# Performance work log

Hardware: AMD Instinct MI355X
Metric: run time of the kernel (lower is better)

The kernel has to match this reference:

```python
import jax, jax.numpy as jnp
import numpy as np

B, C, N, K = 8, 128, 16384, 8


def setup_inputs() -> dict:
    key = jax.random.key(0)
    ks = jax.random.split(key, 20)
    s = 1.0 / np.sqrt(C)
    def mat(k_, shape, scale):
        return jax.random.normal(k_, shape, jnp.float32) * scale
    return {
        "x": jax.random.normal(ks[0], (B, C, N, 1), jnp.float32),
        "logits": jax.random.normal(ks[1], (B, N), jnp.float32),
        "Wq1": mat(ks[2], (C, C), s), "Wk1": mat(ks[3], (C, C), s), "Wv1": mat(ks[4], (C, C), s),
        "Wq2": mat(ks[5], (C, C), s), "Wk2": mat(ks[6], (C, C), s), "Wv2": mat(ks[7], (C, C), s),
        "Wq3": mat(ks[8], (C, C), s), "Wk3": mat(ks[9], (C, C), s), "Wv3": mat(ks[10], (C, C), s),
        "ln_w": jnp.ones((C,), jnp.float32), "ln_b": jnp.zeros((C,), jnp.float32),
        "conv0_w": mat(ks[11], (C, C), s), "conv0_b": jnp.zeros((C,), jnp.float32),
        "bn_w": jnp.ones((C,), jnp.float32), "bn_b": jnp.zeros((C,), jnp.float32),
        "fc1_w": mat(ks[12], (C // 2, C), s), "fc1_b": jnp.zeros((C // 2,), jnp.float32),
        "fc2_w": mat(ks[13], (C, C // 2), 1.0 / np.sqrt(C // 2)), "fc2_b": jnp.zeros((C,), jnp.float32),
        "k": K,
    }


def _transformer(f, Wq, Wk, Wv):
    # f: [B, C, n] ; 1x1 convs over channel dim
    q = jnp.einsum('oc,bcn->bon', Wq, f)
    kk = jnp.einsum('oc,bcn->bon', Wk, f)
    v = jnp.einsum('oc,bcn->bon', Wv, f)
    temp = jnp.sqrt(jnp.asarray(f.shape[1], f.dtype))
    attn = jax.nn.softmax(jnp.einsum('bcn,bdn->bcd', q / temp, kk), axis=-1)  # [B,C,C]
    return jnp.einsum('bcd,bdn->bcn', attn, v)


def _layernorm_over_c(f, w, b):
    # f: [B, C, n]; original transposes to [B, n, C], LayerNorm(C, eps=1e-6), back
    ft = jnp.swapaxes(f, 1, 2)
    mu = ft.mean(-1, keepdims=True)
    var = ft.var(-1, keepdims=True)
    ft = (ft - mu) * jax.lax.rsqrt(var + 1e-6) * w + b
    return jnp.swapaxes(ft, 1, 2)


def reference(x, logits, Wq1, Wk1, Wv1, Wq2, Wk2, Wv2, Wq3, Wk3, Wv3,
              ln_w, ln_b, conv0_w, conv0_b, bn_w, bn_b, fc1_w, fc1_b, fc2_w, fc2_b, k):
    # --- tanh-threshold binning into k buckets ---
    w = jnp.tanh(logits)                       # [B, N]
    flag = 2.0 / k
    lows = -1.0 + flag * jnp.arange(k, dtype=x.dtype)   # [k]
    highs = lows + flag
    wb = w[None, :, :]                         # [1, B, N]
    # transforto0_1: in (l, r], and original zeros stay zero
    masks = ((wb > lows[:, None, None]) & (wb <= highs[:, None, None]) & (wb != 0)).astype(x.dtype)  # [k,B,N]
    nums = masks.sum(-1)                       # [k, B]
    nums = jnp.where(nums == 0, 1.0, nums)

    x2 = x[..., 0]                             # [B, C, N]
    # masked segment pooling (mean per bin), no channel-broadcast repeat
    pooled = jnp.einsum('bcn,kbn->bck', x2, masks)        # [B, C, k]
    feature = pooled / nums.T[:, None, :]                 # [B, C, k]

    # --- three tiny attention blocks with residual + LN ---
    for Wq, Wk, Wv in ((Wq1, Wk1, Wv1), (Wq2, Wk2, Wv2), (Wq3, Wk3, Wv3)):
        out = _transformer(feature, Wq, Wk, Wv) + feature
        feature = _layernorm_over_c(out, ln_w, ln_b)

    # --- scatter-add reconstruction: sum_i mask_i*x + mask_i*level_i ---
    total = masks.sum(0)                                  # [B, N]
    recon = x2 * total[:, None, :] + jnp.einsum('bck,kbn->bcn', feature, masks)
    result = recon[..., None]                             # [B, C, N, 1]

    # --- SE block ---
    mu_i = result.mean(axis=(2, 3), keepdims=True)
    var_i = result.var(axis=(2, 3), keepdims=True)
    h = (result - mu_i) * jax.lax.rsqrt(var_i + 1e-5)     # InstanceNorm2d
    mu_b = h.mean(axis=(0, 2, 3), keepdims=True)
    var_b = h.var(axis=(0, 2, 3), keepdims=True)
    h = (h - mu_b) * jax.lax.rsqrt(var_b + 1e-5)          # BatchNorm2d (batch stats)
    h = h * bn_w[None, :, None, None] + bn_b[None, :, None, None]
    h = jax.nn.gelu(h, approximate=False)
    conv = jnp.einsum('oc,bcnp->bonp', conv0_w, h) + conv0_b[None, :, None, None]
    sq = conv.reshape(conv.shape[0], conv.shape[1], -1).mean(-1)   # [B, C]
    f1 = jax.nn.gelu(sq @ fc1_w.T + fc1_b, approximate=False)
    f2 = jax.nn.sigmoid(f1 @ fc2_w.T + fc2_b)
    return conv * f2[:, :, None, None]
```

## Files before the change

kernel.cpp:

```cpp
#include <hip/hip_runtime.h>
#include <math.h>

#define Bdim 8
#define Cdim 128
#define Ndim 16384
#define Kdim 8

typedef __attribute__((ext_vector_type(8))) short short8;
typedef __attribute__((ext_vector_type(4))) float f32x4;

__device__ __forceinline__ unsigned rne16(float x) {
  unsigned u = __float_as_uint(x);
  return (u + 0x7FFFu + ((u >> 16) & 1u)) >> 16;
}

__global__ void __launch_bounds__(256) k_prep(
    const float* __restrict__ W, unsigned short* __restrict__ Wh,
    unsigned short* __restrict__ Wl, unsigned short* __restrict__ Whs,
    unsigned short* __restrict__ Wls,
    const float* __restrict__ p0, const float* __restrict__ p1, const float* __restrict__ p2,
    const float* __restrict__ p3, const float* __restrict__ p4, const float* __restrict__ p5,
    const float* __restrict__ p6, const float* __restrict__ p7, const float* __restrict__ p8,
    unsigned short* __restrict__ Wbf, int* __restrict__ cnt, float* __restrict__ gmean) {
  int blk = blockIdx.x, t = threadIdx.x;
  if (blk < 64) {
    int idx = blk * 256 + t;
    int o = idx >> 7, c = idx & 127;
    float v = W[idx];
    unsigned u = __float_as_uint(v);
    unsigned rh = (u + 0x7FFFu + ((u >> 16) & 1u)) & 0xFFFF0000u;
    float vh = __uint_as_float(rh);
    float r = v - vh;
    unsigned u2 = __float_as_uint(r);
    unsigned rl = (u2 + 0x7FFFu + ((u2 >> 16) & 1u)) >> 16;
    unsigned short hs = (unsigned short)(rh >> 16);
    unsigned short ls = (unsigned short)rl;
    Wh[idx] = hs;
    Wl[idx] = ls;
    int pos = o * 128 + (((c >> 3) ^ (o & 7)) << 3) + (c & 7);
    Whs[pos] = hs;
    Wls[pos] = ls;
    if (blk == 0 && t < Bdim * Kdim) cnt[t] = 0;
    if (blk < 4) gmean[blk * 256 + t] = 0.f;
  } else {
    int m = (blk - 64) >> 6;
    int i = ((blk - 64) & 63) * 256 + t;
    const float* mp = m == 0 ? p0 : m == 1 ? p1 : m == 2 ? p2 : m == 3 ? p3 : m == 4 ? p4
                    : m == 5 ? p5 : m == 6 ? p6 : m == 7 ? p7 : p8;
    Wbf[m * 16384 + i] = (unsigned short)rne16(mp[i]);
  }
}

__global__ void __launch_bounds__(256) k_bin(const float* __restrict__ logits,
                                             signed char* __restrict__ kbin,
                                             int* __restrict__ cnt) {
  __shared__ int h[Kdim];
  int tid = threadIdx.x;
  if (tid < Kdim) h[tid] = 0;
  __syncthreads();
  int idx = blockIdx.x * 256 + tid;
  int b = idx >> 14;
  float w = tanhf(logits[idx]);
  int kb = -1;
#pragma unroll
  for (int j = 0; j < Kdim; ++j) {
    float lo = -1.0f + 0.25f * (float)j;
    float hi = lo + 0.25f;
    if (w > lo && w <= hi && w != 0.0f) kb = j;
  }
  kbin[idx] = (signed char)kb;
  if (kb >= 0) atomicAdd(&h[kb], 1);
  __syncthreads();
  if (tid < Kdim) atomicAdd(&cnt[b * Kdim + tid], h[tid]);
}

__global__ void __launch_bounds__(256) k_pool(const float* __restrict__ x,
                                              const signed char* __restrict__ kbin,
                                              float* __restrict__ pooled,
                                              float* __restrict__ sxx) {
  int bc = blockIdx.x;
  int b = bc >> 7;
  const float4* xr = (const float4*)(x + (size_t)bc * Ndim);
  const char4* kr = (const char4*)(kbin + b * Ndim);
  float acc[Kdim];
#pragma unroll
  for (int j = 0; j < Kdim; ++j) acc[j] = 0.f;
  float s2 = 0.f;
  int tid = threadIdx.x;
  for (int n4 = tid; n4 < Ndim / 4; n4 += 256) {
    float4 v = xr[n4];
    char4 kb = kr[n4];
    float ve[4] = {v.x, v.y, v.z, v.w};
    signed char ke[4] = {kb.x, kb.y, kb.z, kb.w};
#pragma unroll
    for (int e = 0; e < 4; ++e) {
      float xv = ve[e];
      int kv = ke[e];
      if (kv >= 0) s2 += xv * xv;
#pragma unroll
      for (int j = 0; j < Kdim; ++j) acc[j] += (kv == j) ? xv : 0.f;
    }
  }
#pragma unroll
  for (int off = 32; off > 0; off >>= 1) {
#pragma unroll
    for (int j = 0; j < Kdim; ++j) acc[j] += __shfl_down(acc[j], off);
    s2 += __shfl_down(s2, off);
  }
  __shared__ float red[4][Kdim + 1];
  int wv = tid >> 6, ln = tid & 63;
  if (ln == 0) {
#pragma unroll
    for (int j = 0; j < Kdim; ++j) red[wv][j] = acc[j];
    red[wv][Kdim] = s2;
  }
  __syncthreads();
  if (tid < Kdim) pooled[bc * Kdim + tid] = red[0][tid] + red[1][tid] + red[2][tid] + red[3][tid];
  if (tid == Kdim) sxx[bc] = red[0][Kdim] + red[1][Kdim] + red[2][Kdim] + red[3][Kdim];
}

__global__ void __launch_bounds__(256) k_warm(const unsigned short* __restrict__ Wbf,
                                              float* __restrict__ dummy) {
  int g = blockIdx.x >> 3;
  int t = threadIdx.x;
  int idx = g * 256 + t;
  uint4 v = ((const uint4*)Wbf)[idx];
  float s = (float)(v.x ^ v.y ^ v.z ^ v.w);
#pragma unroll
  for (int off = 32; off > 0; off >>= 1) s += __shfl_down(s, off);
  if ((t & 63) == 0) dummy[blockIdx.x * 4 + (t >> 6)] = s;
}

__global__ void __launch_bounds__(1024) k_xform(
    const float* __restrict__ pooled, const int* __restrict__ cnt,
    const float* __restrict__ sxx, const unsigned short* __restrict__ Wbf,
    const float* __restrict__ ln_w, const float* __restrict__ ln_b,
    float* __restrict__ feat, float* __restrict__ mu_i, float* __restrict__ rs_i,
    float* __restrict__ ratio) {
  __shared__ float f_l[Kdim][132], q_l[Kdim][132], kk_l[Kdim][132], v_l[Kdim][132];
  __shared__ unsigned short fTh[16][132], fTl[16][132];
  __shared__ float part[Kdim][Kdim][Cdim];
  __shared__ float pm[Kdim][Cdim], ps[Kdim][Cdim];
  __shared__ float lnw_l[Cdim], lnb_l[Cdim];
  __shared__ float cnt_raw[Kdim], cnt_div[Kdim];
  __shared__ float redA[Kdim][2], redB[Kdim][2];
  int b = blockIdx.x, tid = threadIdx.x;
  int c_ = tid & 127, h_ = tid >> 7;
  int o8 = tid >> 3, j8 = tid & 7;
  int wid = tid >> 6, lane = tid & 63;
  int l15 = lane & 15, lg = lane >> 4;
  const float inv_temp = 0.08838834764831845f;

  if (tid < Kdim) {
    int cc = cnt[b * Kdim + tid];
    cnt_raw[tid] = (float)cc;
    cnt_div[tid] = (float)(cc == 0 ? 1 : cc);
  }
  if (tid >= 128 && tid < 256) lnw_l[tid - 128] = ln_w[tid - 128];
  if (tid >= 256 && tid < 384) lnb_l[tid - 256] = ln_b[tid - 256];
  __syncthreads();
  {
    float fv = pooled[(b * Cdim + o8) * Kdim + j8] / cnt_div[j8];
    f_l[j8][o8] = fv;
    unsigned hi = rne16(fv);
    fTh[j8][o8] = (unsigned short)hi;
    fTl[j8][o8] = (unsigned short)rne16(fv - __uint_as_float(hi << 16));
  }
  float t_carry = 0.f;
  float sv[16];
  float mloc = 0.f;
  for (int layer = 0; layer < 3; ++layer) {
    if (layer > 0) {
      float S1 = redA[h_][0] + redA[h_][1];
      float S2 = redB[h_][0] + redB[h_][1];
      float mu = S1 * (1.f / Cdim);
      float var = S2 * (1.f / Cdim) - mu * mu;
      float rs = rsqrtf(var + 1e-6f);
      float fv = (t_carry - mu) * rs * lnw_l[c_] + lnb_l[c_];
      f_l[h_][c_] = fv;
      unsigned hi = rne16(fv);
      fTh[h_][c_] = (unsigned short)hi;
      fTl[h_][c_] = (unsigned short)rne16(fv - __uint_as_float(hi << 16));
    }
    __syncthreads();
    for (int job = wid; job < 24; job += 16) {
      int m = job >> 3, ot = job & 7;
      const unsigned short* A = Wbf + (size_t)(layer * 3 + m) * 16384 + (ot * 16 + l15) * 128;
      f32x4 acc = (f32x4){0.f, 0.f, 0.f, 0.f};
#pragma unroll
      for (int ks = 0; ks < 4; ++ks) {
        int kbase = ks * 32 + lg * 8;
        short8 a = *(const short8*)(A + kbase);
        short8 bh = *(const short8*)&fTh[l15][kbase];
        short8 bl = *(const short8*)&fTl[l15][kbase];
        acc = __builtin_amdgcn_mfma_f32_16x16x32_bf16(a, bh, acc, 0, 0, 0);
        acc = __builtin_amdgcn_mfma_f32_16x16x32_bf16(a, bl, acc, 0, 0, 0);
      }
      if (l15 < 8) {
#pragma unroll
        for (int r = 0; r < 4; ++r) {
          int o = ot * 16 + lg * 4 + r;
          float v = acc[r];
          if (m == 0) q_l[l15][o] = v * inv_temp;
          else if (m == 1) kk_l[l15][o] = v;
          else v_l[l15][o] = v;
        }
      }
    }
    __syncthreads();
    {
      int d0 = h_ * 16;
      float qv[8];
#pragma unroll
      for (int j = 0; j < 8; ++j) qv[j] = q_l[j][c_];
#pragma unroll
      for (int dd = 0; dd < 16; ++dd) sv[dd] = 0.f;
#pragma unroll
      for (int j = 0; j < 8; ++j) {
#pragma unroll
        for (int d4 = 0; d4 < 4; ++d4) {
          float4 k4 = *(const float4*)&kk_l[j][d0 + d4 * 4];
          sv[d4 * 4 + 0] = fmaf(qv[j], k4.x, sv[d4 * 4 + 0]);
          sv[d4 * 4 + 1] = fmaf(qv[j], k4.y, sv[d4 * 4 + 1]);
          sv[d4 * 4 + 2] = fmaf(qv[j], k4.z, sv[d4 * 4 + 2]);
          sv[d4 * 4 + 3] = fmaf(qv[j], k4.w, sv[d4 * 4 + 3]);
        }
      }
      mloc = sv[0];
#pragma unroll
      for (int dd = 1; dd < 16; ++dd) mloc = fmaxf(mloc, sv[dd]);
      float sl = 0.f;
#pragma unroll
      for (int dd = 0; dd < 16; ++dd) {
        sv[dd] = expf(sv[dd] - mloc);
        sl += sv[dd];
      }
      pm[h_][c_] = mloc;
      ps[h_][c_] = sl;
    }
    __syncthreads();
    {
      float M = pm[0][c_];
#pragma unroll
      for (int hh = 1; hh < 8; ++hh) M = fmaxf(M, pm[hh][c_]);
      float S = 0.f;
#pragma unroll
      for (int hh = 0; hh < 8; ++hh) S += ps[hh][c_] * expf(pm[hh][c_] - M);
      float fac = expf(mloc - M) / S;
#pragma unroll
      for (int dd = 0; dd < 16; ++dd) sv[dd] *= fac;
      int d0 = h_ * 16;
#pragma unroll
      for (int j = 0; j < 8; ++j) {
        float po = 0.f;
#pragma unroll
        for (int d4 = 0; d4 < 4; ++d4) {
          float4 v4 = *(const float4*)&v_l[j][d0 + d4 * 4];
          po = fmaf(sv[d4 * 4 + 0], v4.x, po);
          po = fmaf(sv[d4 * 4 + 1], v4.y, po);
          po = fmaf(sv[d4 * 4 + 2], v4.z, po);
          po = fmaf(sv[d4 * 4 + 3], v4.w, po);
        }
        part[h_][j][c_] = po;
      }
    }
    __syncthreads();
    {
      float t = f_l[h_][c_];
#pragma unroll
      for (int hh = 0; hh < 8; ++hh) t += part[hh][h_][c_];
      t_carry = t;
      float s1 = t, s2 = t * t;
#pragma unroll
      for (int off = 32; off > 0; off >>= 1) {
        s1 += __shfl_xor(s1, off);
        s2 += __shfl_xor(s2, off);
      }
      int wv = (tid >> 6) & 1;
      if ((tid & 63) == 0) { redA[h_][wv] = s1; redB[h_][wv] = s2; }
    }
    __syncthreads();
  }
  {
    float S1 = redA[h_][0] + redA[h_][1];
    float S2 = redB[h_][0] + redB[h_][1];
    float mu = S1 * (1.f / Cdim);
    float var = S2 * (1.f / Cdim) - mu * mu;
    float rs = rsqrtf(var + 1e-6f);
    f_l[h_][c_] = (t_carry - mu) * rs * lnw_l[c_] + lnb_l[c_];
  }
  __syncthreads();
  if (tid < Cdim) {
    int c = tid;
    float S1 = 0.f, S2c = 0.f;
#pragma unroll
    for (int j = 0; j < Kdim; ++j) {
      float pl = pooled[(b * Cdim + c) * Kdim + j];
      float fe = f_l[j][c];
      feat[(b * Cdim + c) * Kdim + j] = fe;
      S1 += pl + cnt_raw[j] * fe;
      S2c += 2.f * pl * fe + cnt_raw[j] * fe * fe;
    }
    float S2 = sxx[b * Cdim + c] + S2c;
    float mu = S1 * (1.f / Ndim);
    float var = S2 * (1.f / Ndim) - mu * mu;
    float rs = rsqrtf(var + 1e-5f);
    mu_i[b * Cdim + c] = mu;
    rs_i[b * Cdim + c] = rs;
    ratio[b * Cdim + c] = var * rs * rs;
  }
}

__global__ void k_alpha(const float* __restrict__ mu_i, const float* __restrict__ rs_i,
                        const float* __restrict__ ratio, const float* __restrict__ bn_w,
                        const float* __restrict__ bn_b, float* __restrict__ alpha,
                        float* __restrict__ beta) {
  int c = threadIdx.x;
  float vb = 0.f;
  for (int b = 0; b < Bdim; ++b) vb += ratio[b * Cdim + c];
  vb *= (1.f / Bdim);
  float rsb = rsqrtf(vb + 1e-5f);
  float w = bn_w[c], bb = bn_b[c];
  for (int b = 0; b < Bdim; ++b) {
    float a = rs_i[b * Cdim + c] * rsb * w;
    alpha[b * Cdim + c] = a;
    beta[b * Cdim + c] = bb - mu_i[b * Cdim + c] * a;
  }
}

__global__ void __launch_bounds__(256) k_gpack(
    const float* __restrict__ x, const signed char* __restrict__ kbin,
    const float* __restrict__ feat,
    const float* __restrict__ mu_i, const float* __restrict__ rs_i,
    const float* __restrict__ ratio, const float* __restrict__ bn_w,
    const float* __restrict__ bn_b, unsigned short* __restrict__ gpack,
    float* __restrict__ gsum) {
  __shared__ unsigned short xg[Cdim][132];
  __shared__ float feat_l[Cdim][Kdim];
  __shared__ float al_l[Cdim], be_l[Cdim];
  __shared__ signed char kb_l[128];
  int tile = blockIdx.x;
  int b = tile >> 7, nb = tile & 127;
  int n0 = nb * 128;
  int t = threadIdx.x;
  for (int idx = t; idx < Cdim * Kdim; idx += 256)
    ((float*)feat_l)[idx] = feat[b * Cdim * Kdim + idx];
  if (t < 128) {
    int c = t;
    float vb = 0.f;
#pragma unroll
    for (int bb = 0; bb < Bdim; ++bb) vb += ratio[bb * Cdim + c];
    vb *= (1.f / Bdim);
    float rsb = rsqrtf(vb + 1e-5f);
    float a = rs_i[b * Cdim + c] * rsb * bn_w[c];
    al_l[c] = a;
    be_l[c] = bn_b[c] - mu_i[b * Cdim + c] * a;
    kb_l[c] = kbin[b * Ndim + n0 + c];
  }
  __syncthreads();
#pragma unroll 4
  for (int it = 0; it < 16; ++it) {
    int idx = it * 256 + t;
    int q = idx & 31, c = idx >> 5;
    float4 xv = *(const float4*)(x + ((size_t)(b * Cdim + c)) * Ndim + n0 + q * 4);
    float a = al_l[c], be = be_l[c];
    float xe[4] = {xv.x, xv.y, xv.z, xv.w};
    unsigned short rr[4];
#pragma unroll
    for (int e = 0; e < 4; ++e) {
      int kb = kb_l[q * 4 + e];
      float rec = (kb >= 0) ? (xe[e] + feat_l[c][kb]) : 0.0f;
      float h = fmaf(a, rec, be);
      float g = 0.5f * h * (1.0f + erff(h * 0.7071067811865475244f));
      rr[e] = (unsigned short)rne16(g);
    }
    *(ushort4*)&xg[c][q * 4] = make_ushort4(rr[0], rr[1], rr[2], rr[3]);
  }
  __syncthreads();
  {
    int c = t >> 1, half = t & 1;
    float s = 0.f;
#pragma unroll 8
    for (int i = 0; i < 64; ++i) {
      unsigned us = xg[c][half * 64 + i];
      s += __uint_as_float(us << 16);
    }
    s += __shfl_xor(s, 1);
    if (half == 0) atomicAdd(&gsum[b * Cdim + c], s);
  }
  unsigned short* tb = gpack + (size_t)tile * 16384;
#pragma unroll 2
  for (int it = 0; it < 8; ++it) {
    int idx = it * 256 + t;
    int cg = idx & 15, n = idx >> 4;
    unsigned u32s[4];
#pragma unroll
    for (int p = 0; p < 4; ++p) {
      unsigned lo = xg[cg * 8 + 2 * p][n];
      unsigned hi = xg[cg * 8 + 2 * p + 1][n];
      u32s[p] = lo | (hi << 16);
    }
    int g = cg ^ (n & 7);
    *(uint4*)(tb + n * 128 + g * 8) = make_uint4(u32s[0], u32s[1], u32s[2], u32s[3]);
  }
}

__global__ void __launch_bounds__(256) k_gmean(
    const float* __restrict__ x, const signed char* __restrict__ kbin,
    const float* __restrict__ feat, const float* __restrict__ alpha,
    const float* __restrict__ beta, float* __restrict__ gmean) {
  int bc = blockIdx.x;
  int b = bc >> 7;
  __shared__ float fl[Kdim];
  int tid = threadIdx.x;
  if (tid < Kdim) fl[tid] = feat[bc * Kdim + tid];
  __syncthreads();
  float a = alpha[bc], be = beta[bc];
  const float4* xr = (const float4*)(x + (size_t)bc * Ndim);
  const char4* kr = (const char4*)(kbin + b * Ndim);
  float s = 0.f;
  for (int n4 = tid; n4 < Ndim / 4; n4 += 256) {
    float4 v = xr[n4];
    char4 kb = kr[n4];
    float ve[4] = {v.x, v.y, v.z, v.w};
    signed char ke[4] = {kb.x, kb.y, kb.z, kb.w};
#pragma unroll
    for (int e = 0; e < 4; ++e) {
      int kv = ke[e];
      float rec = 0.f;
#pragma unroll
      for (int j = 0; j < Kdim; ++j) rec += (kv == j) ? (ve[e] + fl[j]) : 0.f;
      float h = fmaf(a, rec, be);
      s += 0.5f * h * (1.0f + erff(h * 0.7071067811865475244f));
    }
  }
#pragma unroll
  for (int off = 32; off > 0; off >>= 1) s += __shfl_down(s, off);
  __shared__ float red[4];
  int wv = tid >> 6;
  if ((tid & 63) == 0) red[wv] = s;
  __syncthreads();
  if (tid == 0) gmean[bc] = (red[0] + red[1] + red[2] + red[3]) * (1.0f / Ndim);
}

__global__ void __launch_bounds__(128) k_mlp(const float* __restrict__ gmean,
                                             const float* __restrict__ W,
                                             const float* __restrict__ conv_b,
                                             const float* __restrict__ fc1w,
                                             const float* __restrict__ fc1b,
                                             const float* __restrict__ fc2w,
                                             const float* __restrict__ fc2b,
                                             float inv,
                                             float* __restrict__ f2g) {
  __shared__ float gm[Cdim];
  __shared__ float sq[Cdim];
  __shared__ float f1[64];
  int b = blockIdx.x, tid = threadIdx.x;
  gm[tid] = gmean[b * Cdim + tid] * inv;
  __syncthreads();
  float a = conv_b[tid];
  const float* wr = W + tid * Cdim;
  for (int c = 0; c < Cdim; ++c) a = fmaf(wr[c], gm[c], a);
  sq[tid] = a;
  __syncthreads();
  if (tid < 64) {
    float a1 = fc1b[tid];
    for (int c = 0; c < Cdim; ++c) a1 = fmaf(fc1w[tid * Cdim + c], sq[c], a1);
    f1[tid] = 0.5f * a1 * (1.0f + erff(a1 * 0.7071067811865475244f));
  }
  __syncthreads();
  float a2 = fc2b[tid];
  for (int i = 0; i < 64; ++i) a2 = fmaf(fc2w[tid * 64 + i], f1[i], a2);
  f2g[b * Cdim + tid] = 1.0f / (1.0f + expf(-a2));
}

__global__ void __launch_bounds__(1024) k_conv_g(
    const unsigned short* __restrict__ gpack,
    const unsigned short* __restrict__ Whs, const unsigned short* __restrict__ Wls,
    const float* __restrict__ bias, const float* __restrict__ f2g,
    float* __restrict__ out) {
  __shared__ unsigned short Whl[16384];
  __shared__ unsigned short Wll[16384];
  __shared__ unsigned short Bb[2][16384];
  __shared__ float bi_l[Cdim], f2_l[Cdim];
  int t = threadIdx.x;
  int blk = blockIdx.x;
  int b = blk >> 5;
  int tile0 = blk * 4;
  if (t < 128) {
    bi_l[t] = bias[t];
    f2_l[t] = f2g[b * Cdim + t];
  }
  {
    const uint4* gw = (const uint4*)Whs;
    const uint4* gl = (const uint4*)Wls;
    const uint4* gb = (const uint4*)(gpack + (size_t)tile0 * 16384);
    uint4* lw = (uint4*)Whl;
    uint4* ll = (uint4*)Wll;
    uint4* lb = (uint4*)Bb[0];
    lw[t] = gw[t]; lw[t + 1024] = gw[t + 1024];
    ll[t] = gl[t]; ll[t + 1024] = gl[t + 1024];
    lb[t] = gb[t]; lb[t + 1024] = gb[t + 1024];
  }
  __syncthreads();
  int w = t >> 6, lane = t & 63;
  int wo = (w & 1) * 64, wn = (w >> 1) * 16;
  int l15 = lane & 15, lg = lane >> 4;
  int nrow = wn + l15;
  int brow = nrow * 128;
  int bswz = nrow & 7;
  int cur = 0;
  for (int tt = 0; tt < 4; ++tt) {
    uint4 rb0, rb1;
    if (tt < 3) {
      const uint4* gb = (const uint4*)(gpack + (size_t)(tile0 + tt + 1) * 16384);
      rb0 = gb[t];
      rb1 = gb[t + 1024];
    }
    f32x4 acc[4];
#pragma unroll
    for (int of = 0; of < 4; ++of) acc[of] = (f32x4){0.f, 0.f, 0.f, 0.f};
#pragma unroll
    for (int kb = 0; kb < 4; ++kb) {
      int g = kb * 4 + lg;
      short8 bb = *(const short8*)&Bb[cur][brow + ((g ^ bswz) << 3)];
#pragma unroll
      for (int of = 0; of < 4; ++of) {
        int o = wo + of * 16 + l15;
        int apos = o * 128 + ((g ^ (o & 7)) << 3);
        short8 ah = *(const short8*)&Whl[apos];
        short8 al_ = *(const short8*)&Wll[apos];
        acc[of] = __builtin_amdgcn_mfma_f32_16x16x32_bf16(ah, bb, acc[of], 0, 0, 0);
        acc[of] = __builtin_amdgcn_mfma_f32_16x16x32_bf16(al_, bb, acc[of], 0, 0, 0);
      }
    }
    __syncthreads();
    if (tt < 3) {
      uint4* lb = (uint4*)Bb[cur ^ 1];
      lb[t] = rb0;
      lb[t + 1024] = rb1;
    }
    __syncthreads();
    int n0 = ((tile0 + tt) & 127) * 128;
#pragma unroll
    for (int of = 0; of < 4; ++of) {
#pragma unroll
      for (int r = 0; r < 4; ++r) {
        int o = wo + of * 16 + lg * 4 + r;
        out[((size_t)(b * Cdim + o)) * Ndim + n0 + wn + l15] =
            (acc[of][r] + bi_l[o]) * f2_l[o];
      }
    }
    cur ^= 1;
  }
}

__global__ void __launch_bounds__(512, 4) k_conv_x(
    const float* __restrict__ x, const signed char* __restrict__ kbin,
    const float* __restrict__ feat, const float* __restrict__ alpha,
    const float* __restrict__ beta,
    const unsigned short* __restrict__ Wh, const unsigned short* __restrict__ Wl,
    const float* __restrict__ bias, const float* __restrict__ f2g,
    float* __restrict__ out) {
  __shared__ unsigned g_hl[Cdim][132];
  __shared__ float feat_l[Cdim][Kdim];
  __shared__ float al_l[Cdim], be_l[Cdim], f2_l[Cdim], bi_l[Cdim];
  __shared__ signed char kb_l[128];
  int bx = blockIdx.x;
  int b = bx >> 7, nb = bx & 127;
  int n0 = nb * 128;
  int tid = threadIdx.x;
  for (int idx = tid; idx < Cdim * Kdim; idx += 512)
    ((float*)feat_l)[idx] = feat[b * Cdim * Kdim + idx];
  if (tid < Cdim) {
    al_l[tid] = alpha[b * Cdim + tid];
    be_l[tid] = beta[b * Cdim + tid];
    f2_l[tid] = f2g[b * Cdim + tid];
    bi_l[tid] = bias[tid];
  }
  if (tid >= 256 && tid < 384) kb_l[tid - 256] = kbin[b * Ndim + n0 + (tid - 256)];
  __syncthreads();
  for (int idx = tid; idx < Cdim * 32; idx += 512) {
    int c = idx >> 5, q4 = idx & 31;
    float4 xv = *(const float4*)(x + ((size_t)(b * Cdim + c)) * Ndim + n0 + q4 * 4);
    float a = al_l[c], be = be_l[c];
    float xe[4] = {xv.x, xv.y, xv.z, xv.w};
    unsigned r[4];
#pragma unroll
    for (int e = 0; e < 4; ++e) {
      int kb = kb_l[q4 * 4 + e];
      float rec = (kb >= 0) ? (xe[e] + feat_l[c][kb]) : 0.0f;
      float h = fmaf(a, rec, be);
      float g = 0.5f * h * (1.0f + erff(h * 0.7071067811865475244f));
      unsigned u = __float_as_uint(g);
      unsigned rh = (u + 0x7FFFu + ((u >> 16) & 1u)) & 0xFFFF0000u;
      float rr = g - __uint_as_float(rh);
      unsigned u2 = __float_as_uint(rr);
      unsigned rl = (u2 + 0x7FFFu + ((u2 >> 16) & 1u)) >> 16;
      r[e] = rh | rl;
    }
    int p4 = (q4 * 4) ^ (((c >> 3) & 1) << 4);
    *(uint4*)&g_hl[c][p4] = make_uint4(r[0], r[1], r[2], r[3]);
  }
  __syncthreads();
  int wid = tid >> 6, lane = tid & 63;
  int wo = (wid & 1) * 64;
  int wn = (wid >> 1) * 32;
  int l15 = lane & 15, lg = lane >> 4;
  f32x4 acc[4][2];
#pragma unroll
  for (int of = 0; of < 4; ++of)
#pragma unroll
    for (int nf = 0; nf < 2; ++nf) acc[of][nf] = (f32x4){0.f, 0.f, 0.f, 0.f};
#pragma unroll 2
  for (int kb = 0; kb < 4; ++kb) {
    int kbase = kb * 32 + lg * 8;
    short8 ah[4], alo[4];
#pragma unroll
    for (int of = 0; of < 4; ++of) {
      int o = wo + of * 16 + l15;
      ah[of] = *(const short8*)(Wh + o * Cdim + kbase);
      alo[of] = *(const short8*)(Wl + o * Cdim + kbase);
    }
#pragma unroll
    for (int nf = 0; nf < 2; ++nf) {
      int n = wn + nf * 16 + l15;
      int par = lg & 1;
      short8 bh, bl;
#pragma unroll
      for (int j = 0; j < 8; ++j) {
        unsigned u = g_hl[kbase + j][n ^ (par << 4)];
        bh[j] = (short)(u >> 16);
        bl[j] = (short)(u & 0xFFFFu);
      }
#pragma unroll
      for (int of = 0; of < 4; ++of) {
        acc[of][nf] = __builtin_amdgcn_mfma_f32_16x16x32_bf16(ah[of], bh, acc[of][nf], 0, 0, 0);
        acc[of][nf] = __builtin_amdgcn_mfma_f32_16x16x32_bf16(ah[of], bl, acc[of][nf], 0, 0, 0);
        acc[of][nf] = __builtin_amdgcn_mfma_f32_16x16x32_bf16(alo[of], bh, acc[of][nf], 0, 0, 0);
      }
    }
  }
#pragma unroll
  for (int of = 0; of < 4; ++of) {
#pragma unroll
    for (int nf = 0; nf < 2; ++nf) {
#pragma unroll
      for (int r = 0; r < 4; ++r) {
        int o = wo + of * 16 + lg * 4 + r;
        int n = wn + nf * 16 + l15;
        out[((size_t)(b * Cdim + o)) * Ndim + n0 + n] = (acc[of][nf][r] + bi_l[o]) * f2_l[o];
      }
    }
  }
}

extern "C" void kernel_launch(void* const* d_in, const int* in_sizes, int n_in,
                              void* d_out, int out_size, void* d_ws, size_t ws_size,
                              hipStream_t stream) {
  const float* x = (const float*)d_in[0];
  const float* logits = (const float*)d_in[1];
  const float* Wq1 = (const float*)d_in[2];
  const float* Wk1 = (const float*)d_in[3];
  const float* Wv1 = (const float*)d_in[4];
  const float* Wq2 = (const float*)d_in[5];
  const float* Wk2 = (const float*)d_in[6];
  const float* Wv2 = (const float*)d_in[7];
  const float* Wq3 = (const float*)d_in[8];
  const float* Wk3 = (const float*)d_in[9];
  const float* Wv3 = (const float*)d_in[10];
  const float* ln_w = (const float*)d_in[11];
  const float* ln_b = (const float*)d_in[12];
  const float* conv0_w = (const float*)d_in[13];
  const float* conv0_b = (const float*)d_in[14];
  const float* bn_w = (const float*)d_in[15];
  const float* bn_b = (const float*)d_in[16];
  const float* fc1_w = (const float*)d_in[17];
  const float* fc1_b = (const float*)d_in[18];
  const float* fc2_w = (const float*)d_in[19];
  const float* fc2_b = (const float*)d_in[20];
  float* out = (float*)d_out;

  char* p = (char*)d_ws;
  auto alloc = [&](size_t bytes) {
    char* r = p;
    p += (bytes + 255) & ~(size_t)255;
    return r;
  };
  signed char* kbin = (signed char*)alloc(Bdim * Ndim);
  int* cnt = (int*)alloc(Bdim * Kdim * 4);
  float* pooled = (float*)alloc(Bdim * Cdim * Kdim * 4);
  float* sxx = (float*)alloc(Bdim * Cdim * 4);
  float* feat = (float*)alloc(Bdim * Cdim * Kdim * 4);
  float* mu_i = (float*)alloc(Bdim * Cdim * 4);
  float* rs_i = (float*)alloc(Bdim * Cdim * 4);
  float* ratio = (float*)alloc(Bdim * Cdim * 4);
  float* alpha = (float*)alloc(Bdim * Cdim * 4);
  float* beta = (float*)alloc(Bdim * Cdim * 4);
  unsigned short* Wh = (unsigned short*)alloc(Cdim * Cdim * 2);
  unsigned short* Wlo = (unsigned short*)alloc(Cdim * Cdim * 2);
  unsigned short* Whs = (unsigned short*)alloc(Cdim * Cdim * 2);
  unsigned short* Wls = (unsigned short*)alloc(Cdim * Cdim * 2);
  unsigned short* Wbf = (unsigned short*)alloc(9 * Cdim * Cdim * 2);
  float* f2g = (float*)alloc(Bdim * Cdim * 4);
  float* gmean = (float*)alloc(Bdim * Cdim * 4);
  float* warmdummy = (float*)alloc(576 * 4 * 4);
  unsigned short* gpack = (unsigned short*)alloc((size_t)Bdim * Cdim * Ndim * 2);
  bool fast = ((size_t)(p - (char*)d_ws) <= ws_size);

  k_prep<<<640, 256, 0, stream>>>(conv0_w, Wh, Wlo, Whs, Wls,
                                  Wq1, Wk1, Wv1, Wq2, Wk2, Wv2, Wq3, Wk3, Wv3,
                                  Wbf, cnt, gmean);
  k_bin<<<Bdim * Ndim / 256, 256, 0, stream>>>(logits, kbin, cnt);
  k_pool<<<Bdim * Cdim, 256, 0, stream>>>(x, kbin, pooled, sxx);
  k_warm<<<576, 256, 0, stream>>>(Wbf, warmdummy);
  k_xform<<<Bdim, 1024, 0, stream>>>(pooled, cnt, sxx, Wbf, ln_w, ln_b,
                                     feat, mu_i, rs_i, ratio);
  if (fast) {
    k_gpack<<<Bdim * 128, 256, 0, stream>>>(x, kbin, feat, mu_i, rs_i, ratio, bn_w, bn_b,
                                            gpack, gmean);
    k_mlp<<<Bdim, 128, 0, stream>>>(gmean, conv0_w, conv0_b, fc1_w, fc1_b, fc2_w, fc2_b,
                                    1.0f / Ndim, f2g);
    k_conv_g<<<256, 1024, 0, stream>>>(gpack, Whs, Wls, conv0_b, f2g, out);
  } else {
    k_alpha<<<1, 128, 0, stream>>>(mu_i, rs_i, ratio, bn_w, bn_b, alpha, beta);
    k_gmean<<<Bdim * Cdim, 256, 0, stream>>>(x, kbin, feat, alpha, beta, gmean);
    k_mlp<<<Bdim, 128, 0, stream>>>(gmean, conv0_w, conv0_b, fc1_w, fc1_b, fc2_w, fc2_b,
                                    1.0f, f2g);
    k_conv_x<<<Bdim * (Ndim / 128), 512, 0, stream>>>(x, kbin, feat, alpha, beta, Wh, Wlo,
                                                      conv0_b, f2g, out);
  }
}
```

Baseline: 120.8 us.

## Fuse GELU recompute into conv kernel, drop bf16 staging buffer

```diff
diff --git a/kernel.cpp b/kernel.cpp
--- a/kernel.cpp
+++ b/kernel.cpp
@@ -15,13 +15,12 @@
 }
 
 __global__ void __launch_bounds__(256) k_prep(
-    const float* __restrict__ W, unsigned short* __restrict__ Wh,
-    unsigned short* __restrict__ Wl, unsigned short* __restrict__ Whs,
+    const float* __restrict__ W, unsigned short* __restrict__ Whs,
     unsigned short* __restrict__ Wls,
     const float* __restrict__ p0, const float* __restrict__ p1, const float* __restrict__ p2,
     const float* __restrict__ p3, const float* __restrict__ p4, const float* __restrict__ p5,
     const float* __restrict__ p6, const float* __restrict__ p7, const float* __restrict__ p8,
-    unsigned short* __restrict__ Wbf, int* __restrict__ cnt, float* __restrict__ gmean) {
+    unsigned short* __restrict__ Wbf, int* __restrict__ cnt) {
   int blk = blockIdx.x, t = threadIdx.x;
   if (blk < 64) {
     int idx = blk * 256 + t;
@@ -33,15 +32,10 @@
     float r = v - vh;
     unsigned u2 = __float_as_uint(r);
     unsigned rl = (u2 + 0x7FFFu + ((u2 >> 16) & 1u)) >> 16;
-    unsigned short hs = (unsigned short)(rh >> 16);
-    unsigned short ls = (unsigned short)rl;
-    Wh[idx] = hs;
-    Wl[idx] = ls;
     int pos = o * 128 + (((c >> 3) ^ (o & 7)) << 3) + (c & 7);
-    Whs[pos] = hs;
-    Wls[pos] = ls;
+    Whs[pos] = (unsigned short)(rh >> 16);
+    Wls[pos] = (unsigned short)rl;
     if (blk == 0 && t < Bdim * Kdim) cnt[t] = 0;
-    if (blk < 4) gmean[blk * 256 + t] = 0.f;
   } else {
     int m = (blk - 64) >> 6;
     int i = ((blk - 64) & 63) * 256 + t;
@@ -328,83 +322,6 @@
   }
 }
 
-__global__ void __launch_bounds__(256) k_gpack(
-    const float* __restrict__ x, const signed char* __restrict__ kbin,
-    const float* __restrict__ feat,
-    const float* __restrict__ mu_i, const float* __restrict__ rs_i,
-    const float* __restrict__ ratio, const float* __restrict__ bn_w,
-    const float* __restrict__ bn_b, unsigned short* __restrict__ gpack,
-    float* __restrict__ gsum) {
-  __shared__ unsigned short xg[Cdim][132];
-  __shared__ float feat_l[Cdim][Kdim];
-  __shared__ float al_l[Cdim], be_l[Cdim];
-  __shared__ signed char kb_l[128];
-  int tile = blockIdx.x;
-  int b = tile >> 7, nb = tile & 127;
-  int n0 = nb * 128;
-  int t = threadIdx.x;
-  for (int idx = t; idx < Cdim * Kdim; idx += 256)
-    ((float*)feat_l)[idx] = feat[b * Cdim * Kdim + idx];
-  if (t < 128) {
-    int c = t;
-    float vb = 0.f;
-#pragma unroll
-    for (int bb = 0; bb < Bdim; ++bb) vb += ratio[bb * Cdim + c];
-    vb *= (1.f / Bdim);
-    float rsb = rsqrtf(vb + 1e-5f);
-    float a = rs_i[b * Cdim + c] * rsb * bn_w[c];
-    al_l[c] = a;
-    be_l[c] = bn_b[c] - mu_i[b * Cdim + c] * a;
-    kb_l[c] = kbin[b * Ndim + n0 + c];
-  }
-  __syncthreads();
-#pragma unroll 4
-  for (int it = 0; it < 16; ++it) {
-    int idx = it * 256 + t;
-    int q = idx & 31, c = idx >> 5;
-    float4 xv = *(const float4*)(x + ((size_t)(b * Cdim + c)) * Ndim + n0 + q * 4);
-    float a = al_l[c], be = be_l[c];
-    float xe[4] = {xv.x, xv.y, xv.z, xv.w};
-    unsigned short rr[4];
-#pragma unroll
-    for (int e = 0; e < 4; ++e) {
-      int kb = kb_l[q * 4 + e];
-      float rec = (kb >= 0) ? (xe[e] + feat_l[c][kb]) : 0.0f;
-      float h = fmaf(a, rec, be);
-      float g = 0.5f * h * (1.0f + erff(h * 0.7071067811865475244f));
-      rr[e] = (unsigned short)rne16(g);
-    }
-    *(ushort4*)&xg[c][q * 4] = make_ushort4(rr[0], rr[1], rr[2], rr[3]);
-  }
-  __syncthreads();
-  {
-    int c = t >> 1, half = t & 1;
-    float s = 0.f;
-#pragma unroll 8
-    for (int i = 0; i < 64; ++i) {
-      unsigned us = xg[c][half * 64 + i];
-      s += __uint_as_float(us << 16);
-    }
-    s += __shfl_xor(s, 1);
-    if (half == 0) atomicAdd(&gsum[b * Cdim + c], s);
-  }
-  unsigned short* tb = gpack + (size_t)tile * 16384;
-#pragma unroll 2
-  for (int it = 0; it < 8; ++it) {
-    int idx = it * 256 + t;
-    int cg = idx & 15, n = idx >> 4;
-    unsigned u32s[4];
-#pragma unroll
-    for (int p = 0; p < 4; ++p) {
-      unsigned lo = xg[cg * 8 + 2 * p][n];
-      unsigned hi = xg[cg * 8 + 2 * p + 1][n];
-      u32s[p] = lo | (hi << 16);
-    }
-    int g = cg ^ (n & 7);
-    *(uint4*)(tb + n * 128 + g * 8) = make_uint4(u32s[0], u32s[1], u32s[2], u32s[3]);
-  }
-}
-
 __global__ void __launch_bounds__(256) k_gmean(
     const float* __restrict__ x, const signed char* __restrict__ kbin,
     const float* __restrict__ feat, const float* __restrict__ alpha,
@@ -450,13 +367,12 @@
                                              const float* __restrict__ fc1b,
                                              const float* __restrict__ fc2w,
                                              const float* __restrict__ fc2b,
-                                             float inv,
                                              float* __restrict__ f2g) {
   __shared__ float gm[Cdim];
   __shared__ float sq[Cdim];
   __shared__ float f1[64];
   int b = blockIdx.x, tid = threadIdx.x;
-  gm[tid] = gmean[b * Cdim + tid] * inv;
+  gm[tid] = gmean[b * Cdim + tid];
   __syncthreads();
   float a = conv_b[tid];
   const float* wr = W + tid * Cdim;
@@ -474,48 +390,80 @@
   f2g[b * Cdim + tid] = 1.0f / (1.0f + expf(-a2));
 }
 
-__global__ void __launch_bounds__(1024) k_conv_g(
-    const unsigned short* __restrict__ gpack,
+__global__ void __launch_bounds__(1024) k_convf(
+    const float* __restrict__ x, const signed char* __restrict__ kbin,
+    const float* __restrict__ feat, const float* __restrict__ alpha,
+    const float* __restrict__ beta,
     const unsigned short* __restrict__ Whs, const unsigned short* __restrict__ Wls,
     const float* __restrict__ bias, const float* __restrict__ f2g,
     float* __restrict__ out) {
   __shared__ unsigned short Whl[16384];
   __shared__ unsigned short Wll[16384];
-  __shared__ unsigned short Bb[2][16384];
-  __shared__ float bi_l[Cdim], f2_l[Cdim];
+  __shared__ unsigned short Bg[2][Cdim][132];
+  __shared__ float feat_l[Cdim][Kdim];
+  __shared__ float al_l[Cdim], be_l[Cdim], bi_l[Cdim], f2_l[Cdim];
   int t = threadIdx.x;
   int blk = blockIdx.x;
   int b = blk >> 5;
   int tile0 = blk * 4;
-  if (t < 128) {
-    bi_l[t] = bias[t];
-    f2_l[t] = f2g[b * Cdim + t];
-  }
   {
     const uint4* gw = (const uint4*)Whs;
     const uint4* gl = (const uint4*)Wls;
-    const uint4* gb = (const uint4*)(gpack + (size_t)tile0 * 16384);
-    uint4* lw = (uint4*)Whl;
-    uint4* ll = (uint4*)Wll;
-    uint4* lb = (uint4*)Bb[0];
-    lw[t] = gw[t]; lw[t + 1024] = gw[t + 1024];
-    ll[t] = gl[t]; ll[t + 1024] = gl[t + 1024];
-    lb[t] = gb[t]; lb[t + 1024] = gb[t + 1024];
+    ((uint4*)Whl)[t] = gw[t];
+    ((uint4*)Whl)[t + 1024] = gw[t + 1024];
+    ((uint4*)Wll)[t] = gl[t];
+    ((uint4*)Wll)[t + 1024] = gl[t + 1024];
+  }
+  ((float*)feat_l)[t] = feat[b * Cdim * Kdim + t];
+  if (t < 128) {
+    al_l[t] = alpha[b * Cdim + t];
+    be_l[t] = beta[b * Cdim + t];
+    bi_l[t] = bias[t];
+    f2_l[t] = f2g[b * Cdim + t];
+  }
+  int q = t & 31;
+  int c0 = t >> 5;
+  float4 xv[4];
+  char4 kc;
+  {
+    int nb = tile0 & 127;
+#pragma unroll
+    for (int i = 0; i < 4; ++i)
+      xv[i] = *(const float4*)(x + ((size_t)(b * Cdim + c0 + i * 32)) * Ndim + nb * 128 + q * 4);
+    kc = *(const char4*)(kbin + b * Ndim + nb * 128 + q * 4);
+  }
+  __syncthreads();
+  {
+#pragma unroll
+    for (int i = 0; i < 4; ++i) {
+      int c = c0 + i * 32;
+      float a = al_l[c], be = be_l[c];
+      float xe[4] = {xv[i].x, xv[i].y, xv[i].z, xv[i].w};
+      signed char ke[4] = {kc.x, kc.y, kc.z, kc.w};
+      unsigned short rr[4];
+#pragma unroll
+      for (int e = 0; e < 4; ++e) {
+        float rec = (ke[e] >= 0) ? (xe[e] + feat_l[c][ke[e]]) : 0.0f;
+        float h = fmaf(a, rec, be);
+        float g = 0.5f * h * (1.0f + erff(h * 0.7071067811865475244f));
+        rr[e] = (unsigned short)rne16(g);
+      }
+      *(ushort4*)&Bg[0][c][q * 4] = make_ushort4(rr[0], rr[1], rr[2], rr[3]);
+    }
   }
   __syncthreads();
   int w = t >> 6, lane = t & 63;
   int wo = (w & 1) * 64, wn = (w >> 1) * 16;
   int l15 = lane & 15, lg = lane >> 4;
   int nrow = wn + l15;
-  int brow = nrow * 128;
-  int bswz = nrow & 7;
   int cur = 0;
   for (int tt = 0; tt < 4; ++tt) {
-    uint4 rb0, rb1;
     if (tt < 3) {
-      const uint4* gb = (const uint4*)(gpack + (size_t)(tile0 + tt + 1) * 16384);
-      rb0 = gb[t];
-      rb1 = gb[t + 1024];
+      int nb = (tile0 + tt + 1) & 127;
+#pragma unroll
+      for (int i = 0; i < 4; ++i)
+        xv[i] = *(const float4*)(x + ((size_t)(b * Cdim + c0 + i * 32)) * Ndim + nb * 128 + q * 4);
+      kc = *(const char4*)(kbin + b * Ndim + nb * 128 + q * 4);
     }
     f32x4 acc[4];
 #pragma unroll
@@ -523,7 +471,10 @@
 #pragma unroll
     for (int kb = 0; kb < 4; ++kb) {
       int g = kb * 4 + lg;
-      short8 bb = *(const short8*)&Bb[cur][brow + ((g ^ bswz) << 3)];
+      int kbase = g * 8;
+      short8 bb;
+#pragma unroll
+      for (int j = 0; j < 8; ++j) bb[j] = (short)Bg[cur][kbase + j][nrow];
 #pragma unroll
       for (int of = 0; of < 4; ++of) {
         int o = wo + of * 16 + l15;
@@ -536,9 +487,22 @@
     }
     __syncthreads();
     if (tt < 3) {
-      uint4* lb = (uint4*)Bb[cur ^ 1];
-      lb[t] = rb0;
-      lb[t + 1024] = rb1;
+#pragma unroll
+      for (int i = 0; i < 4; ++i) {
+        int c = c0 + i * 32;
+        float a = al_l[c], be = be_l[c];
+        float xe[4] = {xv[i].x, xv[i].y, xv[i].z, xv[i].w};
+        signed char ke[4] = {kc.x, kc.y, kc.z, kc.w};
+        unsigned short rr[4];
+#pragma unroll
+        for (int e = 0; e < 4; ++e) {
+          float rec = (ke[e] >= 0) ? (xe[e] + feat_l[c][ke[e]]) : 0.0f;
+          float h = fmaf(a, rec, be);
+          float g = 0.5f * h * (1.0f + erff(h * 0.7071067811865475244f));
+          rr[e] = (unsigned short)rne16(g);
+        }
+        *(ushort4*)&Bg[cur ^ 1][c][q * 4] = make_ushort4(rr[0], rr[1], rr[2], rr[3]);
+      }
     }
     __syncthreads();
     int n0 = ((tile0 + tt) & 127) * 128;
@@ -552,106 +516,6 @@
       }
     }
     cur ^= 1;
-  }
-}
-
-__global__ void __launch_bounds__(512, 4) k_conv_x(
-    const float* __restrict__ x, const signed char* __restrict__ kbin,
-    const float* __restrict__ feat, const float* __restrict__ alpha,
-    const float* __restrict__ beta,
-    const unsigned short* __restrict__ Wh, const unsigned short* __restrict__ Wl,
-    const float* __restrict__ bias, const float* __restrict__ f2g,
-    float* __restrict__ out) {
-  __shared__ unsigned g_hl[Cdim][132];
-  __shared__ float feat_l[Cdim][Kdim];
-  __shared__ float al_l[Cdim], be_l[Cdim], f2_l[Cdim], bi_l[Cdim];
-  __shared__ signed char kb_l[128];
-  int bx = blockIdx.x;
-  int b = bx >> 7, nb = bx & 127;
-  int n0 = nb * 128;
-  int tid = threadIdx.x;
-  for (int idx = tid; idx < Cdim * Kdim; idx += 512)
-    ((float*)feat_l)[idx] = feat[b * Cdim * Kdim + idx];
-  if (tid < Cdim) {
-    al_l[tid] = alpha[b * Cdim + tid];
-    be_l[tid] = beta[b * Cdim + tid];
-    f2_l[tid] = f2g[b * Cdim + tid];
-    bi_l[tid] = bias[tid];
-  }
-  if (tid >= 256 && tid < 384) kb_l[tid - 256] = kbin[b * Ndim + n0 + (tid - 256)];
-  __syncthreads();
-  for (int idx = tid; idx < Cdim * 32; idx += 512) {
-    int c = idx >> 5, q4 = idx & 31;
-    float4 xv = *(const float4*)(x + ((size_t)(b * Cdim + c)) * Ndim + n0 + q4 * 4);
-    float a = al_l[c], be = be_l[c];
-    float xe[4] = {xv.x, xv.y, xv.z, xv.w};
-    unsigned r[4];
-#pragma unroll
-    for (int e = 0; e < 4; ++e) {
-      int kb = kb_l[q4 * 4 + e];
-      float rec = (kb >= 0) ? (xe[e] + feat_l[c][kb]) : 0.0f;
-      float h = fmaf(a, rec, be);
-      float g = 0.5f * h * (1.0f + erff(h * 0.7071067811865475244f));
-      unsigned u = __float_as_uint(g);
-      unsigned rh = (u + 0x7FFFu + ((u >> 16) & 1u)) & 0xFFFF0000u;
-      float rr = g - __uint_as_float(rh);
-      unsigned u2 = __float_as_uint(rr);
-      unsigned rl = (u2 + 0x7FFFu + ((u2 >> 16) & 1u)) >> 16;
-      r[e] = rh | rl;
-    }
-    int p4 = (q4 * 4) ^ (((c >> 3) & 1) << 4);
-    *(uint4*)&g_hl[c][p4] = make_uint4(r[0], r[1], r[2], r[3]);
-  }
-  __syncthreads();
-  int wid = tid >> 6, lane = tid & 63;
-  int wo = (wid & 1) * 64;
-  int wn = (wid >> 1) * 32;
-  int l15 = lane & 15, lg = lane >> 4;
-  f32x4 acc[4][2];
-#pragma unroll
-  for (int of = 0; of < 4; ++of)
-#pragma unroll
-    for (int nf = 0; nf < 2; ++nf) acc[of][nf] = (f32x4){0.f, 0.f, 0.f, 0.f};
-#pragma unroll 2
-  for (int kb = 0; kb < 4; ++kb) {
-    int kbase = kb * 32 + lg * 8;
-    short8 ah[4], alo[4];
-#pragma unroll
-    for (int of = 0; of < 4; ++of) {
-      int o = wo + of * 16 + l15;
-      ah[of] = *(const short8*)(Wh + o * Cdim + kbase);
-      alo[of] = *(const short8*)(Wl + o * Cdim + kbase);
-    }
-#pragma unroll
-    for (int nf = 0; nf < 2; ++nf) {
-      int n = wn + nf * 16 + l15;
-      int par = lg & 1;
-      short8 bh, bl;
-#pragma unroll
-      for (int j = 0; j < 8; ++j) {
-        unsigned u = g_hl[kbase + j][n ^ (par << 4)];
-        bh[j] = (short)(u >> 16);
-        bl[j] = (short)(u & 0xFFFFu);
-      }
-#pragma unroll
-      for (int of = 0; of < 4; ++of) {
-        acc[of][nf] = __builtin_amdgcn_mfma_f32_16x16x32_bf16(ah[of], bh, acc[of][nf], 0, 0, 0);
-        acc[of][nf] = __builtin_amdgcn_mfma_f32_16x16x32_bf16(ah[of], bl, acc[of][nf], 0, 0, 0);
-        acc[of][nf] = __builtin_amdgcn_mfma_f32_16x16x32_bf16(alo[of], bh, acc[of][nf], 0, 0, 0);
-      }
-    }
-  }
-#pragma unroll
-  for (int of = 0; of < 4; ++of) {
-#pragma unroll
-    for (int nf = 0; nf < 2; ++nf) {
-#pragma unroll
-      for (int r = 0; r < 4; ++r) {
-        int o = wo + of * 16 + lg * 4 + r;
-        int n = wn + nf * 16 + l15;
-        out[((size_t)(b * Cdim + o)) * Ndim + n0 + n] = (acc[of][nf][r] + bi_l[o]) * f2_l[o];
-      }
-    }
   }
 }
 
@@ -697,37 +561,25 @@
   float* ratio = (float*)alloc(Bdim * Cdim * 4);
   float* alpha = (float*)alloc(Bdim * Cdim * 4);
   float* beta = (float*)alloc(Bdim * Cdim * 4);
-  unsigned short* Wh = (unsigned short*)alloc(Cdim * Cdim * 2);
-  unsigned short* Wlo = (unsigned short*)alloc(Cdim * Cdim * 2);
   unsigned short* Whs = (unsigned short*)alloc(Cdim * Cdim * 2);
   unsigned short* Wls = (unsigned short*)alloc(Cdim * Cdim * 2);
   unsigned short* Wbf = (unsigned short*)alloc(9 * Cdim * Cdim * 2);
   float* f2g = (float*)alloc(Bdim * Cdim * 4);
   float* gmean = (float*)alloc(Bdim * Cdim * 4);
   float* warmdummy = (float*)alloc(576 * 4 * 4);
-  unsigned short* gpack = (unsigned short*)alloc((size_t)Bdim * Cdim * Ndim * 2);
-  bool fast = ((size_t)(p - (char*)d_ws) <= ws_size);
-
-  k_prep<<<640, 256, 0, stream>>>(conv0_w, Wh, Wlo, Whs, Wls,
+  (void)ws_size;
+
+  k_prep<<<640, 256, 0, stream>>>(conv0_w, Whs, Wls,
                                   Wq1, Wk1, Wv1, Wq2, Wk2, Wv2, Wq3, Wk3, Wv3,
-                                  Wbf, cnt, gmean);
+                                  Wbf, cnt);
   k_bin<<<Bdim * Ndim / 256, 256, 0, stream>>>(logits, kbin, cnt);
   k_pool<<<Bdim * Cdim, 256, 0, stream>>>(x, kbin, pooled, sxx);
   k_warm<<<576, 256, 0, stream>>>(Wbf, warmdummy);
   k_xform<<<Bdim, 1024, 0, stream>>>(pooled, cnt, sxx, Wbf, ln_w, ln_b,
                                      feat, mu_i, rs_i, ratio);
-  if (fast) {
-    k_gpack<<<Bdim * 128, 256, 0, stream>>>(x, kbin, feat, mu_i, rs_i, ratio, bn_w, bn_b,
-                                            gpack, gmean);
-    k_mlp<<<Bdim, 128, 0, stream>>>(gmean, conv0_w, conv0_b, fc1_w, fc1_b, fc2_w, fc2_b,
-                                    1.0f / Ndim, f2g);
-    k_conv_g<<<256, 1024, 0, stream>>>(gpack, Whs, Wls, conv0_b, f2g, out);
-  } else {
-    k_alpha<<<1, 128, 0, stream>>>(mu_i, rs_i, ratio, bn_w, bn_b, alpha, beta);
-    k_gmean<<<Bdim * Cdim, 256, 0, stream>>>(x, kbin, feat, alpha, beta, gmean);
-    k_mlp<<<Bdim, 128, 0, stream>>>(gmean, conv0_w, conv0_b, fc1_w, fc1_b, fc2_w, fc2_b,
-                                    1.0f, f2g);
-    k_conv_x<<<Bdim * (Ndim / 128), 512, 0, stream>>>(x, kbin, feat, alpha, beta, Wh, Wlo,
-                                                      conv0_b, f2g, out);
-  }
-}
+  k_alpha<<<1, 128, 0, stream>>>(mu_i, rs_i, ratio, bn_w, bn_b, alpha, beta);
+  k_gmean<<<Bdim * Cdim, 256, 0, stream>>>(x, kbin, feat, alpha, beta, gmean);
+  k_mlp<<<Bdim, 128, 0, stream>>>(gmean, conv0_w, conv0_b, fc1_w, fc1_b, fc2_w, fc2_b, f2g);
+  k_convf<<<256, 1024, 0, stream>>>(x, kbin, feat, alpha, beta, Whs, Wls,
+                                    conv0_b, f2g, out);
+}
```

Result: slower. 134.1 us (+11.0%).
